# Optimization experiments

Hardware: AMD Instinct MI355X
Metric: run time of the kernel (lower is better)

Reference implementation:

```python
import jax, jax.numpy as jnp
import numpy as np

B, T, D = 32, 1024, 256
TOP_K = 2
EPS_ADJ = 1e-6
LN_EPS = 1e-5


def setup_inputs() -> dict:
    key = jax.random.key(0)
    ks = jax.random.split(key, 10)
    inp = {
        'x': jax.random.normal(ks[0], (B, T, D), dtype=jnp.float32),
        'mask': jnp.ones((B, T), dtype=jnp.int32),
    }
    # two GCN layers: linear W [D_out, D_in] (torch layout), bias, LayerNorm gamma/beta
    for li in range(2):
        inp[f'W{li}'] = jax.random.normal(ks[1 + 4 * li], (D, D), dtype=jnp.float32) * (1.0 / np.sqrt(D))
        inp[f'b{li}'] = jax.random.normal(ks[2 + 4 * li], (D,), dtype=jnp.float32) * 0.02
        inp[f'g{li}'] = jnp.ones((D,), dtype=jnp.float32)
        inp[f'be{li}'] = jnp.zeros((D,), dtype=jnp.float32)
    return inp


def _layer_norm(x, gamma, beta):
    mu = jnp.mean(x, axis=-1, keepdims=True)
    var = jnp.mean(jnp.square(x - mu), axis=-1, keepdims=True)
    return (x - mu) * jax.lax.rsqrt(var + LN_EPS) * gamma + beta


def _cos_sim(x, maskf):
    x_norm = x / jnp.clip(jnp.linalg.norm(x, axis=-1, keepdims=True), 1e-12)
    sim = jnp.einsum('bid,bjd->bij', x_norm, x_norm)
    return sim * (maskf[:, :, None] * maskf[:, None, :])


def _build_adj(sim, maskf):
    b, t, _ = sim.shape
    eye = jnp.eye(t, dtype=sim.dtype)
    # temporal chain edges + self loops
    base_adj = eye + jnp.eye(t, k=1, dtype=sim.dtype) + jnp.eye(t, k=-1, dtype=sim.dtype)
    # top-k over similarity with diagonal suppressed
    corel = jnp.where(eye[None] == 1, -1.0, sim)
    _, topk_inds = jax.lax.top_k(corel, TOP_K)  # [B, T, K]
    bi = jnp.arange(b)[:, None, None]
    ii = jnp.arange(t)[None, :, None]
    ext = jnp.zeros_like(sim).at[bi, ii, topk_inds].set(1.0)
    ext = jnp.maximum(ext, jnp.swapaxes(ext, 1, 2))
    ext = ext * (maskf[:, :, None] * maskf[:, None, :])
    adj = jnp.clip(base_adj[None] + ext, 0.0, 1.0) * sim + eye[None]
    row_sum = jnp.sum(adj, axis=-1, keepdims=True) + EPS_ADJ
    col_sum = jnp.sum(adj, axis=1, keepdims=True) + EPS_ADJ
    adj = adj / jnp.sqrt(row_sum * col_sum)
    return adj * (maskf[:, :, None] * maskf[:, None, :])


def reference(x, mask, W0, b0, g0, be0, W1, b1, g1, be1):
    maskf = mask.astype(x.dtype)
    sim = _cos_sim(x, maskf)
    adj = _build_adj(sim, maskf)
    params = [(W0, b0, g0, be0), (W1, b1, g1, be1)]
    h = x
    for (W, bb, g, be) in params:
        h = jnp.einsum('bij,bjd->bid', adj, h)
        h = jnp.einsum('bid,od->bio', h, W) + bb
        h = jax.nn.elu(h)
        h = _layer_norm(h, g, be)
        # dropout: identity in eval mode
    return h
```

## Files before the change

### kernel.cpp

```cpp
#include <hip/hip_runtime.h>
#include <math.h>

#define NB 32
#define NT 1024
#define ND 256
#define NROWS (NB*NT)
#define MAXE 64

typedef __attribute__((ext_vector_type(8))) short bf16x8;
typedef __attribute__((ext_vector_type(4))) float f32x4;
typedef unsigned short ushort_t;
typedef unsigned long long u64;

__device__ inline ushort_t f2bf_rn(float f){
  unsigned u = __float_as_uint(f);
  unsigned r = u + 0x7fffu + ((u >> 16) & 1u);
  return (ushort_t)(r >> 16);
}
__device__ inline float bf2f(ushort_t h){
  return __uint_as_float(((unsigned)h) << 16);
}
__device__ inline void ceswap(u64 &a, u64 &b){
  u64 mx = a > b ? a : b;
  u64 mn = a > b ? b : a;
  a = mx; b = mn;
}
__device__ inline u64 umax64(u64 a, u64 b){ return a > b ? a : b; }

__global__ __launch_bounds__(256) void k_norm(const float* __restrict__ x,
                                              float* __restrict__ xn,
                                              ushort_t* __restrict__ xh,
                                              ushort_t* __restrict__ xl){
  int row = blockIdx.x;
  int t = threadIdx.x;
  size_t base = (size_t)row*ND;
  float v = x[base + t];
  float ss = v*v;
  #pragma unroll
  for (int off=32; off; off>>=1) ss += __shfl_xor(ss, off);
  __shared__ float sred[4];
  if ((t & 63) == 0) sred[t>>6] = ss;
  __syncthreads();
  float tot = sred[0] + sred[1] + sred[2] + sred[3];
  float nrm = fmaxf(sqrtf(tot), 1e-12f);
  float res = v / nrm;
  xn[base + t] = res;
  ushort_t hb = f2bf_rn(res);
  float lres = res - bf2f(hb);
  xh[base + t] = hb;
  xl[base + t] = f2bf_rn(lres);
}

__global__ __launch_bounds__(256) void k_wsplit(const float* __restrict__ W0,
                                                const float* __restrict__ W1,
                                                ushort_t* __restrict__ Wh0, ushort_t* __restrict__ Wl0,
                                                ushort_t* __restrict__ Wh1, ushort_t* __restrict__ Wl1){
  int idx = blockIdx.x*256 + threadIdx.x;
  float w0 = W0[idx]; ushort_t h0 = f2bf_rn(w0);
  Wh0[idx] = h0; Wl0[idx] = f2bf_rn(w0 - bf2f(h0));
  float w1 = W1[idx]; ushort_t h1 = f2bf_rn(w1);
  Wh1[idx] = h1; Wl1[idx] = f2bf_rn(w1 - bf2f(h1));
}

__global__ __launch_bounds__(256) void k_sim(const ushort_t* __restrict__ xh,
                                             const ushort_t* __restrict__ xl,
                                             ushort_t* __restrict__ S,
                                             int bat0){
  __shared__ __align__(16) ushort_t lds[2*128*80];
  ushort_t* As  = lds;
  ushort_t* Bsm = lds + 128*80;

  int blk = blockIdx.x;
  int b_local = blk >> 6;
  int b = bat0 + b_local;
  int tt = blk & 63;
  int ti = tt >> 3, tj = tt & 7;
  int i0 = ti*128, j0 = tj*128;

  int t = threadIdx.x;
  int lane = t & 63, wave = t >> 6;
  int wy = wave >> 1, wx = wave & 1;
  int c = lane & 15, q = lane >> 4;

  f32x4 acc[4][4];
  #pragma unroll
  for (int bi=0;bi<4;bi++)
    #pragma unroll
    for (int bj=0;bj<4;bj++) acc[bi][bj] = {0.f,0.f,0.f,0.f};

  size_t rowbA = (size_t)(b*NT + i0);
  size_t rowbB = (size_t)(b*NT + j0);

  for (int p=0; p<3; p++){
    const ushort_t* Ags = (p==1) ? xl : xh;
    const ushort_t* Bgs = (p==2) ? xl : xh;
    const ushort_t* Ag = Ags + rowbA*ND;
    const ushort_t* Bg = Bgs + rowbB*ND;
    for (int kc=0; kc<4; kc++){
      __syncthreads();
      {
        int r0 = t >> 3, seg = t & 7;
        #pragma unroll
        for (int g=0; g<4; g++){
          int r = r0 + g*32;
          float4 va = *(const float4*)&Ag[(size_t)r*ND + kc*64 + seg*8];
          *(float4*)&As[r*80 + seg*8] = va;
          float4 vb = *(const float4*)&Bg[(size_t)r*ND + kc*64 + seg*8];
          *(float4*)&Bsm[r*80 + seg*8] = vb;
        }
      }
      __syncthreads();
      #pragma unroll
      for (int ks=0; ks<2; ks++){
        bf16x8 af[4], bfr[4];
        #pragma unroll
        for (int bi=0;bi<4;bi++)
          af[bi] = *(const bf16x8*)&As[(wy*64 + bi*16 + c)*80 + ks*32 + q*8];
        #pragma unroll
        for (int bj=0;bj<4;bj++)
          bfr[bj] = *(const bf16x8*)&Bsm[(wx*64 + bj*16 + c)*80 + ks*32 + q*8];
        #pragma unroll
        for (int bi=0;bi<4;bi++)
          #pragma unroll
          for (int bj=0;bj<4;bj++)
            acc[bi][bj] = __builtin_amdgcn_mfma_f32_16x16x32_bf16(af[bi], bfr[bj], acc[bi][bj], 0, 0, 0);
      }
    }
  }

  size_t srow0 = (size_t)b_local*NT + i0 + wy*64;
  int col0 = j0 + wx*64;
  #pragma unroll
  for (int bi=0;bi<4;bi++){
    #pragma unroll
    for (int reg=0;reg<4;reg++){
      ushort_t* dst = S + (srow0 + bi*16 + q*4 + reg)*NT + col0;
      #pragma unroll
      for (int bj=0;bj<4;bj++)
        dst[bj*16 + c] = f2bf_rn(acc[bi][bj][reg]);
    }
  }
}

__global__ __launch_bounds__(256) void k_top8(const ushort_t* __restrict__ S,
                                              int4* __restrict__ cand4,
                                              int rowbase){
  int row = blockIdx.x*4 + (threadIdx.x >> 6);
  int lane = threadIdx.x & 63;
  int i = row & 1023;
  const ushort_t* Sr = S + (size_t)row*NT;
  u64 e0 = 0, e1 = 0;
  #pragma unroll
  for (int seg=0; seg<4; seg++){
    int col = seg*256 + lane*4;
    u64 v4 = *(const u64*)&Sr[col];
    #pragma unroll
    for (int m=0;m<4;m++){
      unsigned u = (unsigned)((v4 >> (16*m)) & 0xffffu) << 16;
      unsigned key = u ^ ((unsigned)((int)u >> 31) | 0x80000000u);
      int j = col + m;
      u64 e = ((u64)key << 32) | (unsigned)j;
      if (j == i) e = 0;
      u64 mn = e0 > e ? e : e0;
      e0 = e0 > e ? e0 : e;
      e1 = e1 > mn ? e1 : mn;
    }
  }
  u64 L0 = e0, L1 = e1, L2 = 0, L3 = 0;
  #pragma unroll
  for (int st=1; st<64; st<<=1){
    u64 R0 = __shfl_xor(L0, st), R1 = __shfl_xor(L1, st);
    u64 R2 = __shfl_xor(L2, st), R3 = __shfl_xor(L3, st);
    u64 m0 = umax64(L0, R3), m1 = umax64(L1, R2);
    u64 m2 = umax64(L2, R1), m3 = umax64(L3, R0);
    ceswap(m0, m2); ceswap(m1, m3); ceswap(m0, m1); ceswap(m2, m3);
    L0 = m0; L1 = m1; L2 = m2; L3 = m3;
  }
  if (lane == 0)
    cand4[rowbase + row] = make_int4((int)(unsigned)L0, (int)(unsigned)L1,
                                     (int)(unsigned)L2, (int)(unsigned)L3);
}

__global__ __launch_bounds__(64) void k_refine4(const float* __restrict__ xn,
                                                const int4* __restrict__ cand4,
                                                int2* __restrict__ top2){
  int row = blockIdx.x; int b = row >> 10, i = row & 1023;
  int l = threadIdx.x;
  const float* Xb = xn + (size_t)b*NT*ND;
  float4 xi = *(const float4*)&Xb[(size_t)i*ND + l*4];
  int4 cd = cand4[row];
  int cands[4] = {cd.x, cd.y, cd.z, cd.w};
  double bv1=-1e30, bv2=-1e30; int bi1=0x7fffffff, bi2=0x7fffffff;
  #pragma unroll
  for (int cq=0;cq<4;cq++){
    int j = cands[cq];
    float4 xj = *(const float4*)&Xb[(size_t)j*ND + l*4];
    double p = (double)xi.x*xj.x + (double)xi.y*xj.y
             + (double)xi.z*xj.z + (double)xi.w*xj.w;
    #pragma unroll
    for (int off=32; off; off>>=1) p += __shfl_xor(p, off);
    if (p > bv1 || (p == bv1 && j < bi1)) { bv2=bv1; bi2=bi1; bv1=p; bi1=j; }
    else if (p > bv2 || (p == bv2 && j < bi2)) { bv2=p; bi2=j; }
  }
  if (l == 0) top2[row] = make_int2(bi1, bi2);
}

__global__ __launch_bounds__(256) void k_scatter(const int2* __restrict__ top2,
                                                 unsigned* __restrict__ ext){
  int row = blockIdx.x*256 + threadIdx.x;
  int b = row >> 10, i = row & 1023;
  int2 tp = top2[row];
  unsigned* eb = ext + (size_t)b*NT*32;
  int j1 = tp.x, j2 = tp.y;
  atomicOr(&eb[(size_t)i*32 + (j1>>5)], 1u << (j1&31));
  atomicOr(&eb[(size_t)j1*32 + (i>>5)], 1u << (i&31));
  atomicOr(&eb[(size_t)i*32 + (j2>>5)], 1u << (j2&31));
  atomicOr(&eb[(size_t)j2*32 + (i>>5)], 1u << (i&31));
}

__global__ __launch_bounds__(64) void k_edges(const float* __restrict__ xn,
                                              const unsigned* __restrict__ ext,
                                              int* __restrict__ eidx,
                                              float* __restrict__ eval_,
                                              float* __restrict__ rs,
                                              int* __restrict__ ecnt){
  int row = blockIdx.x; int b = row >> 10, i = row & 1023;
  int l = threadIdx.x;
  const float* Xb = xn + (size_t)b*NT*ND;
  float4 xi = *(const float4*)&Xb[(size_t)i*ND + l*4];
  unsigned word = 0;
  if (l < 32){
    word = ext[((size_t)b*NT + i)*32 + l];
    int js[3] = {i-1, i, i+1};
    #pragma unroll
    for (int qd=0;qd<3;qd++){
      int j = js[qd];
      if (j >= 0 && j < NT && (j>>5) == l) word |= (1u << (j&31));
    }
  }
  float rsum = 0.f; int cnt = 0;
  for (int w=0; w<32; w++){
    unsigned bits = __shfl(word, w);
    while (bits){
      int bit = __ffs(bits) - 1;
      bits &= bits - 1;
      int j = w*32 + bit;
      float4 xj = *(const float4*)&Xb[(size_t)j*ND + l*4];
      float p = xi.x*xj.x + xi.y*xj.y + xi.z*xj.z + xi.w*xj.w;
      #pragma unroll
      for (int off=32; off; off>>=1) p += __shfl_xor(p, off);
      float v = p + ((j==i) ? 1.0f : 0.0f);
      if (l == 0 && cnt < MAXE){
        eidx[(size_t)row*MAXE + cnt] = j;
        eval_[(size_t)row*MAXE + cnt] = v;
      }
      rsum += v; cnt++;
    }
  }
  if (l == 0){ rs[row] = rsum + 1e-6f; ecnt[row] = (cnt < MAXE) ? cnt : MAXE; }
}

__global__ __launch_bounds__(256) void k_wnorm(const int* __restrict__ eidx,
                                               const float* __restrict__ eval_,
                                               const float* __restrict__ rs,
                                               const int* __restrict__ ecnt,
                                               float* __restrict__ wn){
  int row = blockIdx.x*4 + (threadIdx.x >> 6);
  int lane = threadIdx.x & 63;
  int b = row >> 10;
  int n = ecnt[row];
  float rsi = rs[row];
  if (lane < n){
    int j = eidx[(size_t)row*MAXE + lane];
    float v = eval_[(size_t)row*MAXE + lane];
    wn[(size_t)row*MAXE + lane] = v / sqrtf(rsi * rs[b*NT + j]);
  }
}

__global__ __launch_bounds__(256) void k_spmm(const float* __restrict__ hin,
                                              const int* __restrict__ eidx,
                                              const float* __restrict__ wn,
                                              const int* __restrict__ ecnt,
                                              float* __restrict__ hout){
  int row = blockIdx.x*4 + (threadIdx.x >> 6);
  int lane = threadIdx.x & 63;
  int b = row >> 10;
  const float* Hb = hin + (size_t)b*NT*ND;
  int n = ecnt[row];
  const int* ei = eidx + (size_t)row*MAXE;
  const float* we = wn + (size_t)row*MAXE;
  float4 acc = {0.f,0.f,0.f,0.f};
  int e = 0;
  for (; e+2 <= n; e += 2){
    int j0 = ei[e],   j1 = ei[e+1];
    float w0 = we[e], w1 = we[e+1];
    float4 v0 = *(const float4*)&Hb[(size_t)j0*ND + lane*4];
    float4 v1 = *(const float4*)&Hb[(size_t)j1*ND + lane*4];
    acc.x += w0*v0.x; acc.y += w0*v0.y; acc.z += w0*v0.z; acc.w += w0*v0.w;
    acc.x += w1*v1.x; acc.y += w1*v1.y; acc.z += w1*v1.z; acc.w += w1*v1.w;
  }
  if (e < n){
    int j0 = ei[e]; float w0 = we[e];
    float4 v0 = *(const float4*)&Hb[(size_t)j0*ND + lane*4];
    acc.x += w0*v0.x; acc.y += w0*v0.y; acc.z += w0*v0.z; acc.w += w0*v0.w;
  }
  *(float4*)&hout[(size_t)row*ND + lane*4] = acc;
}

__global__ __launch_bounds__(256) void k_dense2(const float* __restrict__ hs,
                                                const ushort_t* __restrict__ Wh,
                                                const ushort_t* __restrict__ Wl,
                                                const float* __restrict__ bias,
                                                const float* __restrict__ gam,
                                                const float* __restrict__ bet,
                                                float* __restrict__ out){
  __shared__ __align__(16) ushort_t Ah[64*72];
  __shared__ __align__(16) ushort_t Al[64*72];
  __shared__ float sums[64*4];
  __shared__ float sqs[64*4];
  __shared__ float muA[64];
  __shared__ float rsA[64];

  int t = threadIdx.x;
  int lane = t & 63, wave = t >> 6;
  int c = lane & 15, q = lane >> 4;
  size_t row0 = (size_t)blockIdx.x * 64;

  f32x4 acc[4][4];
  #pragma unroll
  for (int bi=0;bi<4;bi++)
    #pragma unroll
    for (int bj=0;bj<4;bj++) acc[bi][bj] = {0.f,0.f,0.f,0.f};

  for (int kc=0; kc<4; kc++){
    __syncthreads();
    {
      int r = t >> 2, csg = (t & 3) * 16;
      const float* src = &hs[(row0 + r)*ND + kc*64 + csg];
      float4 f0 = *(const float4*)&src[0];
      float4 f1 = *(const float4*)&src[4];
      float4 f2 = *(const float4*)&src[8];
      float4 f3 = *(const float4*)&src[12];
      float fa[16] = {f0.x,f0.y,f0.z,f0.w, f1.x,f1.y,f1.z,f1.w,
                      f2.x,f2.y,f2.z,f2.w, f3.x,f3.y,f3.z,f3.w};
      bf16x8 h8[2], l8[2];
      #pragma unroll
      for (int g=0; g<2; g++){
        #pragma unroll
        for (int m=0; m<8; m++){
          float f = fa[g*8 + m];
          ushort_t hb = f2bf_rn(f);
          h8[g][m] = (short)hb;
          l8[g][m] = (short)f2bf_rn(f - bf2f(hb));
        }
      }
      *(bf16x8*)&Ah[r*72 + csg]     = h8[0];
      *(bf16x8*)&Ah[r*72 + csg + 8] = h8[1];
      *(bf16x8*)&Al[r*72 + csg]     = l8[0];
      *(bf16x8*)&Al[r*72 + csg + 8] = l8[1];
    }
    __syncthreads();
    #pragma unroll
    for (int ks=0; ks<2; ks++){
      bf16x8 ah[4], al[4], wh[4], wl[4];
      #pragma unroll
      for (int bi=0;bi<4;bi++){
        ah[bi] = *(const bf16x8*)&Ah[(bi*16+c)*72 + ks*32 + q*8];
        al[bi] = *(const bf16x8*)&Al[(bi*16+c)*72 + ks*32 + q*8];
      }
      #pragma unroll
      for (int bj=0;bj<4;bj++){
        size_t wo = (size_t)(wave*64 + bj*16 + c)*ND + kc*64 + ks*32 + q*8;
        wh[bj] = *(const bf16x8*)&Wh[wo];
        wl[bj] = *(const bf16x8*)&Wl[wo];
      }
      #pragma unroll
      for (int bi=0;bi<4;bi++)
        #pragma unroll
        for (int bj=0;bj<4;bj++){
          acc[bi][bj] = __builtin_amdgcn_mfma_f32_16x16x32_bf16(ah[bi], wh[bj], acc[bi][bj], 0, 0, 0);
          acc[bi][bj] = __builtin_amdgcn_mfma_f32_16x16x32_bf16(al[bi], wh[bj], acc[bi][bj], 0, 0, 0);
          acc[bi][bj] = __builtin_amdgcn_mfma_f32_16x16x32_bf16(ah[bi], wl[bj], acc[bi][bj], 0, 0, 0);
        }
    }
  }

  float bv[4], gv[4], tv[4];
  #pragma unroll
  for (int bj=0;bj<4;bj++){
    int col = wave*64 + bj*16 + c;
    bv[bj] = bias[col]; gv[bj] = gam[col]; tv[bj] = bet[col];
  }
  #pragma unroll
  for (int bi=0;bi<4;bi++)
    #pragma unroll
    for (int bj=0;bj<4;bj++)
      #pragma unroll
      for (int reg=0;reg<4;reg++){
        float v = acc[bi][bj][reg] + bv[bj];
        acc[bi][bj][reg] = (v > 0.f) ? v : expm1f(v);
      }

  #pragma unroll
  for (int bi=0;bi<4;bi++)
    #pragma unroll
    for (int reg=0;reg<4;reg++){
      float s = acc[bi][0][reg] + acc[bi][1][reg] + acc[bi][2][reg] + acc[bi][3][reg];
      #pragma unroll
      for (int st=1; st<16; st<<=1) s += __shfl_xor(s, st);
      if (c == 0) sums[(bi*16 + q*4 + reg)*4 + wave] = s;
    }
  __syncthreads();
  if (t < 64){
    float s = sums[t*4] + sums[t*4+1] + sums[t*4+2] + sums[t*4+3];
    muA[t] = s * (1.0f/ND);
  }
  __syncthreads();
  #pragma unroll
  for (int bi=0;bi<4;bi++)
    #pragma unroll
    for (int reg=0;reg<4;reg++){
      float mu = muA[bi*16 + q*4 + reg];
      float ss = 0.f;
      #pragma unroll
      for (int bj=0;bj<4;bj++){ float d = acc[bi][bj][reg] - mu; ss += d*d; }
      #pragma unroll
      for (int st=1; st<16; st<<=1) ss += __shfl_xor(ss, st);
      if (c == 0) sqs[(bi*16 + q*4 + reg)*4 + wave] = ss;
    }
  __syncthreads();
  if (t < 64){
    float ss = sqs[t*4] + sqs[t*4+1] + sqs[t*4+2] + sqs[t*4+3];
    rsA[t] = rsqrtf(ss * (1.0f/ND) + 1e-5f);
  }
  __syncthreads();
  #pragma unroll
  for (int bi=0;bi<4;bi++)
    #pragma unroll
    for (int reg=0;reg<4;reg++){
      int row = bi*16 + q*4 + reg;
      float mu = muA[row], rst = rsA[row];
      #pragma unroll
      for (int bj=0;bj<4;bj++){
        float val = (acc[bi][bj][reg] - mu) * rst * gv[bj] + tv[bj];
        out[(row0 + row)*ND + wave*64 + bj*16 + c] = val;
      }
    }
}

extern "C" void kernel_launch(void* const* d_in, const int* in_sizes, int n_in,
                              void* d_out, int out_size, void* d_ws, size_t ws_size,
                              hipStream_t stream) {
  (void)in_sizes; (void)n_in; (void)out_size; (void)ws_size;
  const float* x   = (const float*)d_in[0];
  const float* W0  = (const float*)d_in[2];
  const float* b0  = (const float*)d_in[3];
  const float* g0  = (const float*)d_in[4];
  const float* be0 = (const float*)d_in[5];
  const float* W1  = (const float*)d_in[6];
  const float* b1  = (const float*)d_in[7];
  const float* g1  = (const float*)d_in[8];
  const float* be1 = (const float*)d_in[9];
  float* out = (float*)d_out;

  char* wsb = (char*)d_ws;
  float* xn = (float*)wsb;
  ushort_t* xh = (ushort_t*)(wsb + (size_t)32*1024*1024);
  ushort_t* xl = (ushort_t*)(wsb + (size_t)48*1024*1024);
  float* hsbuf = (float*)xh;
  char* zc = wsb + (size_t)64*1024*1024;
  ushort_t* S = (ushort_t*)zc;
  unsigned* ext   = (unsigned*)zc;
  int*      eidx  = (int*)(zc + (size_t)4*1024*1024);
  float*    eval_ = (float*)(zc + (size_t)12*1024*1024);
  float*    rs    = (float*)(zc + (size_t)20*1024*1024);
  int*      ecnt  = (int*)(zc + (size_t)21*1024*1024);
  float*    wn    = (float*)(zc + (size_t)22*1024*1024);
  char* zd = wsb + (size_t)98*1024*1024;
  int4* cand4 = (int4*)zd;
  int2* top2  = (int2*)(zd + (size_t)512*1024);
  ushort_t* Wh0 = (ushort_t*)(zd + (size_t)1024*1024);
  ushort_t* Wl0 = Wh0 + 65536;
  ushort_t* Wh1 = Wl0 + 65536;
  ushort_t* Wl1 = Wh1 + 65536;

  k_wsplit<<<256, 256, 0, stream>>>(W0, W1, Wh0, Wl0, Wh1, Wl1);
  k_norm<<<NROWS, 256, 0, stream>>>(x, xn, xh, xl);
  for (int h=0; h<2; h++){
    int bat0 = h*16;
    k_sim<<<1024, 256, 0, stream>>>(xh, xl, S, bat0);
    k_top8<<<4096, 256, 0, stream>>>(S, cand4, bat0*NT);
  }
  k_refine4<<<NROWS, 64, 0, stream>>>(xn, cand4, top2);
  hipMemsetAsync(ext, 0, (size_t)NROWS*32*4, stream);
  k_scatter<<<NROWS/256, 256, 0, stream>>>(top2, ext);
  k_edges<<<NROWS, 64, 0, stream>>>(xn, ext, eidx, eval_, rs, ecnt);
  k_wnorm<<<NROWS/4, 256, 0, stream>>>(eidx, eval_, rs, ecnt, wn);
  k_spmm<<<NROWS/4, 256, 0, stream>>>(x, eidx, wn, ecnt, hsbuf);
  k_dense2<<<NROWS/64, 256, 0, stream>>>(hsbuf, Wh0, Wl0, b0, g0, be0, out);
  k_spmm<<<NROWS/4, 256, 0, stream>>>(out, eidx, wn, ecnt, hsbuf);
  k_dense2<<<NROWS/64, 256, 0, stream>>>(hsbuf, Wh1, Wl1, b1, g1, be1, out);
}
```

Before: 407.2 us.

## Stage similarity GEMM tiles via direct global-to-LDS loads with XOR swizzle

Rewrites the k_sim tile loop so that the hi and lo bf16 parts of both operands are staged together per k-chunk. The three split-precision products now share one load pass instead of three. Loads use global_load_lds with an XOR-swizzled unpadded LDS layout, which avoids register round-trips and bank conflicts. Block indices are also remapped so that neighbouring blocks cover different batches and tiles, for cache locality. LDS use grows, and more fragment registers are live per k-step.

```diff
diff --git a/kernel.cpp b/kernel.cpp
--- a/kernel.cpp
+++ b/kernel.cpp
@@ -26,6 +26,13 @@
   a = mx; b = mn;
 }
 __device__ inline u64 umax64(u64 a, u64 b){ return a > b ? a : b; }
+
+__device__ inline void gld16(const ushort_t* g, ushort_t* l){
+  __builtin_amdgcn_global_load_lds(
+      (const __attribute__((address_space(1))) unsigned int*)(g),
+      (__attribute__((address_space(3))) unsigned int*)(l),
+      16, 0, 0);
+}
 
 __global__ __launch_bounds__(256) void k_norm(const float* __restrict__ x,
                                               float* __restrict__ xn,
@@ -66,11 +73,14 @@
                                              const ushort_t* __restrict__ xl,
                                              ushort_t* __restrict__ S,
                                              int bat0){
-  __shared__ __align__(16) ushort_t lds[2*128*80];
-  ushort_t* As  = lds;
-  ushort_t* Bsm = lds + 128*80;
-
-  int blk = blockIdx.x;
+  __shared__ __align__(16) ushort_t Ahs[128*64];
+  __shared__ __align__(16) ushort_t Als[128*64];
+  __shared__ __align__(16) ushort_t Bhs[128*64];
+  __shared__ __align__(16) ushort_t Bls[128*64];
+
+  int blk0 = blockIdx.x;
+  int blk = (blk0 & 7)*128 + (blk0 >> 3);
+
   int b_local = blk >> 6;
   int b = bat0 + b_local;
   int tt = blk & 63;
@@ -81,6 +91,8 @@
   int lane = t & 63, wave = t >> 6;
   int wy = wave >> 1, wx = wave & 1;
   int c = lane & 15, q = lane >> 4;
+  int lrow = lane >> 3;
+  int sc   = (lane & 7) ^ lrow;
 
   f32x4 acc[4][4];
   #pragma unroll
@@ -90,41 +102,49 @@
 
   size_t rowbA = (size_t)(b*NT + i0);
   size_t rowbB = (size_t)(b*NT + j0);
-
-  for (int p=0; p<3; p++){
-    const ushort_t* Ags = (p==1) ? xl : xh;
-    const ushort_t* Bgs = (p==2) ? xl : xh;
-    const ushort_t* Ag = Ags + rowbA*ND;
-    const ushort_t* Bg = Bgs + rowbB*ND;
-    for (int kc=0; kc<4; kc++){
-      __syncthreads();
-      {
-        int r0 = t >> 3, seg = t & 7;
+  const ushort_t* Agh = xh + rowbA*ND;
+  const ushort_t* Agl = xl + rowbA*ND;
+  const ushort_t* Bgh = xh + rowbB*ND;
+  const ushort_t* Bgl = xl + rowbB*ND;
+
+  for (int kc=0; kc<4; kc++){
+    __syncthreads();
+    int koff = kc*64;
+    #pragma unroll
+    for (int inst=0; inst<4; inst++){
+      int r0 = wave*32 + inst*8;
+      size_t go = (size_t)(r0 + lrow)*ND + koff + sc*8;
+      gld16(Agh + go, &Ahs[r0*64]);
+      gld16(Agl + go, &Als[r0*64]);
+      gld16(Bgh + go, &Bhs[r0*64]);
+      gld16(Bgl + go, &Bls[r0*64]);
+    }
+    __syncthreads();
+
+    #pragma unroll
+    for (int ks=0; ks<2; ks++){
+      bf16x8 ah[4], al[4], bh[4], bl[4];
+      int slot = (ks*4 + q) ^ (c & 7);
+      #pragma unroll
+      for (int bi=0;bi<4;bi++){
+        int row = wy*64 + bi*16 + c;
+        ah[bi] = *(const bf16x8*)&Ahs[row*64 + slot*8];
+        al[bi] = *(const bf16x8*)&Als[row*64 + slot*8];
+      }
+      #pragma unroll
+      for (int bj=0;bj<4;bj++){
+        int row = wx*64 + bj*16 + c;
+        bh[bj] = *(const bf16x8*)&Bhs[row*64 + slot*8];
+        bl[bj] = *(const bf16x8*)&Bls[row*64 + slot*8];
+      }
+      #pragma unroll
+      for (int bi=0;bi<4;bi++)
         #pragma unroll
-        for (int g=0; g<4; g++){
-          int r = r0 + g*32;
-          float4 va = *(const float4*)&Ag[(size_t)r*ND + kc*64 + seg*8];
-          *(float4*)&As[r*80 + seg*8] = va;
-          float4 vb = *(const float4*)&Bg[(size_t)r*ND + kc*64 + seg*8];
-          *(float4*)&Bsm[r*80 + seg*8] = vb;
+        for (int bj=0;bj<4;bj++){
+          acc[bi][bj] = __builtin_amdgcn_mfma_f32_16x16x32_bf16(ah[bi], bh[bj], acc[bi][bj], 0, 0, 0);
+          acc[bi][bj] = __builtin_amdgcn_mfma_f32_16x16x32_bf16(al[bi], bh[bj], acc[bi][bj], 0, 0, 0);
+          acc[bi][bj] = __builtin_amdgcn_mfma_f32_16x16x32_bf16(ah[bi], bl[bj], acc[bi][bj], 0, 0, 0);
         }
-      }
-      __syncthreads();
-      #pragma unroll
-      for (int ks=0; ks<2; ks++){
-        bf16x8 af[4], bfr[4];
-        #pragma unroll
-        for (int bi=0;bi<4;bi++)
-          af[bi] = *(const bf16x8*)&As[(wy*64 + bi*16 + c)*80 + ks*32 + q*8];
-        #pragma unroll
-        for (int bj=0;bj<4;bj++)
-          bfr[bj] = *(const bf16x8*)&Bsm[(wx*64 + bj*16 + c)*80 + ks*32 + q*8];
-        #pragma unroll
-        for (int bi=0;bi<4;bi++)
-          #pragma unroll
-          for (int bj=0;bj<4;bj++)
-            acc[bi][bj] = __builtin_amdgcn_mfma_f32_16x16x32_bf16(af[bi], bfr[bj], acc[bi][bj], 0, 0, 0);
-      }
     }
   }
 
```

Measured after the change: 389.7 us. -4.3%, faster.
